# Kernel tuning notes

Hardware: AMD Instinct MI355X
Metric: run time of the kernel (lower is better)

## Reference

```python
import jax, jax.numpy as jnp
import numpy as np

B, L = 4096, 64
H, E, T, S = 512, 256, 256, 128
CT = T + 3            # context feature dim (term_embedding_dim + 3)
R, V = 4096, 256      # n production rules, n symbols
IN = 2 * E + 2 * T + 6 + H + S  # GRUCell input dim = 1670
NEG = -1e9


def setup_inputs() -> dict:
    key = jax.random.key(0)
    ks = jax.random.split(key, 24)
    sc = 0.02
    inp = {
        "s_tm1": jax.random.normal(ks[0], (B, H), jnp.float32),
        "a_tm1": jax.random.normal(ks[1], (B, E), jnp.float32),
        "p_t": jax.random.normal(ks[2], (B, H + E), jnp.float32),
        "symbol_idx": jax.random.randint(ks[3], (B,), 0, V, jnp.int32),
        "env_emb": jax.random.normal(ks[4], (B, L, CT), jnp.float32),
        "env_len": jax.random.randint(ks[5], (B,), 0, L, jnp.int32),
        "lc_emb": jax.random.normal(ks[6], (B, L, CT), jnp.float32),
        "lc_len": jax.random.randint(ks[7], (B,), 0, L, jnp.int32),
        # parameters
        "symbol_table": jax.random.normal(ks[8], (V, S), jnp.float32) * sc,
        "W1": jax.random.normal(ks[9], (H + CT, H), jnp.float32) * sc,
        "b1": jnp.zeros((H,), jnp.float32),
        "W2": jax.random.normal(ks[10], (H,), jnp.float32) * sc,
        "b2": jnp.zeros((), jnp.float32),
        "W_ih": jax.random.normal(ks[11], (IN, 3 * H), jnp.float32) * sc,
        "W_hh": jax.random.normal(ks[12], (H, 3 * H), jnp.float32) * sc,
        "b_ih": jnp.zeros((3 * H,), jnp.float32),
        "b_hh": jnp.zeros((3 * H,), jnp.float32),
        "Wd": jax.random.normal(ks[13], (H, E), jnp.float32) * sc,
        "bd": jnp.zeros((E,), jnp.float32),
        "rule_table": jax.random.normal(ks[14], (R, E), jnp.float32) * sc,
    }
    return inp


def _context_read(state, emb, length, W1, b1, W2, b2):
    # state: [B,H], emb: [B,L,CT], length: [B] -> context [B,CT]
    x = jnp.concatenate([jnp.broadcast_to(state[:, None, :], emb.shape[:2] + (state.shape[-1],)), emb], axis=-1)
    h = jax.nn.relu(jnp.einsum('blk,kh->blh', x, W1) + b1)      # [B,L,H]
    logit = jnp.einsum('blh,h->bl', h, W2) + b2                  # [B,L]
    mask = jnp.arange(emb.shape[1])[None, :] < length[:, None]
    logit = jnp.where(mask, logit, NEG)
    w = jax.nn.softmax(logit, axis=1)                            # [B,L]
    ctx = jnp.einsum('bl,blc->bc', w, emb)                       # [B,CT]
    # ragged empty-context samples use the zero default_context
    return jnp.where((length > 0)[:, None], ctx, 0.0)


def reference(s_tm1, a_tm1, p_t, symbol_idx, env_emb, env_len, lc_emb, lc_len,
              symbol_table, W1, b1, W2, b2, W_ih, W_hh, b_ih, b_hh, Wd, bd, rule_table):
    n_t = symbol_table[symbol_idx]                               # [B,S]
    ctx_env = _context_read(s_tm1, env_emb, env_len, W1, b1, W2, b2)
    ctx_lc = _context_read(s_tm1, lc_emb, lc_len, W1, b1, W2, b2)
    x = jnp.concatenate([a_tm1, p_t, n_t, ctx_env, ctx_lc], axis=-1)  # [B,IN]
    # torch GRUCell
    gx = x @ W_ih + b_ih                                         # [B,3H]
    gh = s_tm1 @ W_hh + b_hh
    xr, xz, xn = jnp.split(gx, 3, axis=-1)
    hr, hz, hn = jnp.split(gh, 3, axis=-1)
    r = jax.nn.sigmoid(xr + hr)
    z = jax.nn.sigmoid(xz + hz)
    n = jnp.tanh(xn + r * hn)
    h_new = (1.0 - z) * n + z * s_tm1                            # [B,H]
    dec = jnp.tanh(h_new @ Wd + bd)                              # [B,E]
    logits = dec @ rule_table.T                                  # [B,R]
    return logits
```

## Files before the change

### kernel.cpp

```cpp
#include <hip/hip_runtime.h>
#include <hip/hip_bf16.h>
#include <stdint.h>
#include <stddef.h>

#define XP 1696
#define KC 288

#define BIG_G   8192
#define TWO_G   4096
#define ONE_G   2048
#define N_GROUP (BIG_G + TWO_G + ONE_G)
#define N_SLOTI (N_GROUP * 4)

typedef __attribute__((ext_vector_type(8))) short bf16x8;
typedef __attribute__((ext_vector_type(4))) float f32x4;

__device__ __forceinline__ unsigned short f32_bf16(float f) {
    union { float f; unsigned int u; } v; v.f = f;
    unsigned int r = v.u + 0x7FFFu + ((v.u >> 16) & 1u);
    return (unsigned short)(r >> 16);
}
__device__ __forceinline__ float bf16_f32(unsigned short u) {
    union { unsigned int u; float f; } v; v.u = ((unsigned int)u) << 16;
    return v.f;
}

__global__ void tpack_kernel(const float* __restrict__ src, unsigned short* __restrict__ dst,
                             int Ksrc, int Nsrc, int Kp, long total) {
    long idx = (long)blockIdx.x * blockDim.x + threadIdx.x;
    if (idx >= total) return;
    int k = (int)(idx / Nsrc);
    int n = (int)(idx - (long)k * Nsrc);
    float v = (k < Ksrc) ? src[(size_t)k * Nsrc + n] : 0.0f;
    dst[(size_t)n * Kp + k] = f32_bf16(v);
}

__global__ void cvt_kernel(const float* __restrict__ src, unsigned short* __restrict__ dst, int total) {
    int idx = blockIdx.x * blockDim.x + threadIdx.x;
    if (idx < total) dst[idx] = f32_bf16(src[idx]);
}

__global__ void xasm_kernel(const float* __restrict__ a_tm1, const float* __restrict__ p_t,
                            const int* __restrict__ sym, const float* __restrict__ symtab,
                            unsigned short* __restrict__ x_out) {
    int idx = blockIdx.x * blockDim.x + threadIdx.x;
    if (idx >= 4096 * XP) return;
    int b = idx / XP, c = idx - b * XP;
    float v;
    if (c < 256)       v = a_tm1[(size_t)b * 256 + c];
    else if (c < 1024) v = p_t[(size_t)b * 768 + (c - 256)];
    else if (c < 1152) v = symtab[(size_t)sym[b] * 128 + (c - 1024)];
    else if (c < 1670) return;
    else v = 0.0f;
    x_out[idx] = f32_bf16(v);
}

__global__ void sinit_kernel(int* __restrict__ s) {
    int i = blockIdx.x * 256 + threadIdx.x;
    if (i < N_SLOTI) s[i] = -1;
    else if (i < N_SLOTI + 3) s[i] = 0;
}

__global__ void sched_kernel(const int* __restrict__ len_env, const int* __restrict__ len_lc,
                             int* __restrict__ slots) {
    int idx = blockIdx.x * blockDim.x + threadIdx.x;
    if (idx >= 8192) return;
    int b = idx >> 1, wh = idx & 1;
    int len = wh ? len_lc[b] : len_env[b];
    int m = (len + 15) >> 4;
    if (m == 0) m = 1;
    if (m > 4) m = 4;
    int* cursors = slots + N_SLOTI;
    int base;
    if (m >= 3)      { int p = atomicAdd(&cursors[0], 1); base = p * 4; }
    else if (m == 2) { int p = atomicAdd(&cursors[1], 1); base = BIG_G * 4 + (p >> 1) * 4 + (p & 1) * 2; }
    else             { int p = atomicAdd(&cursors[2], 1); base = (BIG_G + TWO_G) * 4 + (p >> 2) * 4 + (p & 3); }
    for (int k = 0; k < m; k++) slots[base + k] = idx * 4 + k;
}

template<int ACT, int OUT_BF16>
__global__ __launch_bounds__(256, 2)
void gemm_bt_kernel(const unsigned short* __restrict__ A,
                    const unsigned short* __restrict__ BT,
                    const float* __restrict__ bias,
                    void* __restrict__ Cout,
                    int M, int N, int K)
{
    __shared__ unsigned short a_lds[128 * 32];
    __shared__ unsigned short b_lds[128 * 32];
    const int tid  = threadIdx.x;
    const int lane = tid & 63;
    const int wave = tid >> 6;
    const int wm = wave >> 1, wn = wave & 1;
    const int row0 = blockIdx.y * 128;
    const int col0 = blockIdx.x * 128;

    f32x4 acc[4][4];
    #pragma unroll
    for (int i = 0; i < 4; i++)
        #pragma unroll
        for (int j = 0; j < 4; j++) acc[i][j] = (f32x4){0.f, 0.f, 0.f, 0.f};

    const int fr = lane & 15;
    const int kk = (lane >> 4) * 8;
    const int srow = (lane >> 2);
    const int scol = (lane & 3) * 8;

    for (int k0 = 0; k0 < K; k0 += 32) {
        __syncthreads();
        #pragma unroll
        for (int j = 0; j < 4; j++) {
            const int c = (wave & 1) * 4 + j;
            const unsigned short* gsrc;
            unsigned short* ldst;
            if (wave < 2) {
                gsrc = A  + (size_t)(row0 + c * 16 + srow) * K + k0 + scol;
                ldst = &a_lds[c * 512];
            } else {
                gsrc = BT + (size_t)(col0 + c * 16 + srow) * K + k0 + scol;
                ldst = &b_lds[c * 512];
            }
            __builtin_amdgcn_global_load_lds(
                (const __attribute__((address_space(1))) void*)gsrc,
                (__attribute__((address_space(3))) void*)ldst, 16, 0, 0);
        }
        __syncthreads();

        bf16x8 af[4], bf[4];
        #pragma unroll
        for (int mt = 0; mt < 4; mt++) af[mt] = *(const bf16x8*)&a_lds[(wm * 64 + mt * 16 + fr) * 32 + kk];
        #pragma unroll
        for (int nt = 0; nt < 4; nt++) bf[nt] = *(const bf16x8*)&b_lds[(wn * 64 + nt * 16 + fr) * 32 + kk];
        #pragma unroll
        for (int mt = 0; mt < 4; mt++)
            #pragma unroll
            for (int nt = 0; nt < 4; nt++)
                acc[mt][nt] = __builtin_amdgcn_mfma_f32_16x16x32_bf16(af[mt], bf[nt], acc[mt][nt], 0, 0, 0);
    }

    const int fq = lane >> 4;
    #pragma unroll
    for (int mt = 0; mt < 4; mt++)
        #pragma unroll
        for (int nt = 0; nt < 4; nt++) {
            int cg = col0 + wn * 64 + nt * 16 + fr;
            float bv = bias ? bias[cg] : 0.0f;
            #pragma unroll
            for (int i = 0; i < 4; i++) {
                int rg = row0 + wm * 64 + mt * 16 + fq * 4 + i;
                float v = acc[mt][nt][i] + bv;
                if (ACT == 1) v = tanhf(v);
                if (OUT_BF16) ((unsigned short*)Cout)[(size_t)rg * N + cg] = f32_bf16(v);
                else          ((float*)Cout)[(size_t)rg * N + cg] = v;
            }
        }
}

__global__ __launch_bounds__(512, 4)
void ctx_kernel(const float* __restrict__ emb_env, const float* __restrict__ emb_lc,
                const int* __restrict__ len_env, const int* __restrict__ len_lc,
                const float* __restrict__ s_proj,
                const unsigned short* __restrict__ W1eT,
                const float* __restrict__ W2, const float* __restrict__ b2,
                const int* __restrict__ slots,
                unsigned short* __restrict__ x_out)
{
    const int g = blockIdx.x;
    const int4 dv = *reinterpret_cast<const int4*>(slots + (size_t)g * 4);
    if (dv.x < 0) return;
    int d[4] = {dv.x, dv.y, dv.z, dv.w};

    __shared__ unsigned short emb_lds[64][296];
    __shared__ float partial_lds[8][64];
    __shared__ float w_lds[64];

    const int tid = threadIdx.x;
    const int lane = tid & 63;
    const int wave = tid >> 6;
    const int fr = lane & 15;
    const int fq = lane >> 4;
    const float b2v = b2[0];

    {
        const int sl = tid >> 7;
        const int t  = tid & 127;
        const int ds = d[sl];
        int nrows = 0;
        const float* src = nullptr;
        if (ds >= 0) {
            int it = ds >> 2, tix = ds & 3;
            int b = it >> 1, wh = it & 1;
            int len = (wh ? len_lc : len_env)[b];
            nrows = len - tix * 16;
            if (nrows > 16) nrows = 16;
            if (nrows < 0) nrows = 0;
            src = (wh ? emb_lc : emb_env) + ((size_t)b * 64 + tix * 16) * 259;
        }
        for (int q = t; q < 16 * 37; q += 128) {
            int r = q / 37, c = 259 + (q - (q / 37) * 37);
            emb_lds[sl * 16 + r][c] = 0;
        }
        const int ndead = (16 - nrows) * 259;
        for (int q = t; q < ndead; q += 128) {
            int r = nrows + q / 259, c = q - (q / 259) * 259;
            emb_lds[sl * 16 + r][c] = 0;
        }
        const int nf4 = (nrows * 259 + 3) >> 2;
        const float4* s4 = reinterpret_cast<const float4*>(src);
        float4 v[9];
        #pragma unroll
        for (int j = 0; j < 9; j++) {
            int q = t + j * 128;
            if (q < nf4) v[j] = s4[q];
        }
        #pragma unroll
        for (int j = 0; j < 9; j++) {
            int q = t + j * 128;
            if (q < nf4) {
                float fv[4] = {v[j].x, v[j].y, v[j].z, v[j].w};
                int e0 = q * 4;
                #pragma unroll
                for (int jj = 0; jj < 4; jj++) {
                    int e = e0 + jj;
                    int r = e / 259;
                    int c = e - r * 259;
                    emb_lds[sl * 16 + r][c] = f32_bf16(fv[jj]);
                }
            }
        }
    }
    __syncthreads();

    f32x4 acc[4][4];
    #pragma unroll
    for (int i = 0; i < 4; i++)
        #pragma unroll
        for (int j = 0; j < 4; j++) acc[i][j] = (f32x4){0.f, 0.f, 0.f, 0.f};

    #pragma unroll
    for (int ks = 0; ks < 9; ks++) {
        bf16x8 bfr[4];
        #pragma unroll
        for (int nt = 0; nt < 4; nt++) {
            int n = wave * 64 + nt * 16 + fr;
            bfr[nt] = *(const bf16x8*)(W1eT + (size_t)n * KC + ks * 32 + fq * 8);
        }
        bf16x8 af[4];
        #pragma unroll
        for (int mt = 0; mt < 4; mt++)
            af[mt] = *(const bf16x8*)&emb_lds[mt * 16 + fr][ks * 32 + fq * 8];
        __builtin_amdgcn_s_setprio(1);
        #pragma unroll
        for (int nt = 0; nt < 4; nt++)
            #pragma unroll
            for (int mt = 0; mt < 4; mt++)
                acc[mt][nt] = __builtin_amdgcn_mfma_f32_16x16x32_bf16(af[mt], bfr[nt], acc[mt][nt], 0, 0, 0);
        __builtin_amdgcn_s_setprio(0);
    }

    int bslot[4];
    #pragma unroll
    for (int mt = 0; mt < 4; mt++) bslot[mt] = d[mt] >= 0 ? (d[mt] >> 3) : -1;

    float wv[4];
    #pragma unroll
    for (int nt = 0; nt < 4; nt++) wv[nt] = W2[wave * 64 + nt * 16 + fr];

    float plog[4][4];
    #pragma unroll
    for (int mt = 0; mt < 4; mt++)
        #pragma unroll
        for (int ii = 0; ii < 4; ii++) plog[mt][ii] = 0.f;
    #pragma unroll
    for (int nt = 0; nt < 4; nt++) {
        int n = wave * 64 + nt * 16 + fr;
        #pragma unroll
        for (int mt = 0; mt < 4; mt++) {
            if (bslot[mt] < 0) continue;
            float sp = s_proj[(size_t)bslot[mt] * 512 + n];
            #pragma unroll
            for (int ii = 0; ii < 4; ii++) {
                float h = acc[mt][nt][ii] + sp;
                h = fmaxf(h, 0.f);
                plog[mt][ii] += h * wv[nt];
            }
        }
    }
    #pragma unroll
    for (int mt = 0; mt < 4; mt++) {
        if (bslot[mt] < 0) continue;
        #pragma unroll
        for (int ii = 0; ii < 4; ii++) {
            float v = plog[mt][ii];
            v += __shfl_xor(v, 1); v += __shfl_xor(v, 2);
            v += __shfl_xor(v, 4); v += __shfl_xor(v, 8);
            if (fr == 0) partial_lds[wave][mt * 16 + fq * 4 + ii] = v;
        }
    }
    __syncthreads();

    if (wave < 4) {
        int dh = d[wave];
        if (dh >= 0 && (dh & 3) == 0) {
            int it = dh >> 2;
            int b = it >> 1, wh = it & 1;
            int len = (wh ? len_lc : len_env)[b];
            int m = (len + 15) >> 4; if (m == 0) m = 1;
            float logit = -1e9f;
            if (lane < 16 * m && lane < len) {
                logit = b2v;
                #pragma unroll
                for (int w = 0; w < 8; w++) logit += partial_lds[w][wave * 16 + lane];
            }
            float mx = logit;
            #pragma unroll
            for (int off = 1; off < 64; off <<= 1) mx = fmaxf(mx, __shfl_xor(mx, off));
            float e = __expf(logit - mx);
            float s = e;
            #pragma unroll
            for (int off = 1; off < 64; off <<= 1) s += __shfl_xor(s, off);
            if (lane < 16 * m) w_lds[wave * 16 + lane] = e / s;
        }
    }
    __syncthreads();

    #pragma unroll
    for (int g4 = 0; g4 < 4; g4++) {
        int dh = d[g4];
        if (dh < 0 || (dh & 3) != 0) continue;
        int it = dh >> 2;
        int b = it >> 1, wh = it & 1;
        int len = (wh ? len_lc : len_env)[b];
        int xoff = wh ? 1411 : 1152;
        if (tid < 259) {
            const int c = tid;
            const int base = g4 * 16;
            float a0 = 0.f, a1 = 0.f, a2 = 0.f, a3 = 0.f;
            int l = 0;
            for (; l + 3 < len; l += 4) {
                a0 += w_lds[base + l]     * bf16_f32(emb_lds[base + l][c]);
                a1 += w_lds[base + l + 1] * bf16_f32(emb_lds[base + l + 1][c]);
                a2 += w_lds[base + l + 2] * bf16_f32(emb_lds[base + l + 2][c]);
                a3 += w_lds[base + l + 3] * bf16_f32(emb_lds[base + l + 3][c]);
            }
            for (; l < len; l++) a0 += w_lds[base + l] * bf16_f32(emb_lds[base + l][c]);
            x_out[(size_t)b * XP + xoff + c] = f32_bf16((a0 + a1) + (a2 + a3));
        }
    }
}

__global__ void gru_kernel(const float* __restrict__ gx, const float* __restrict__ gh,
                           const float* __restrict__ s, unsigned short* __restrict__ h_b) {
    int idx = blockIdx.x * blockDim.x + threadIdx.x;
    if (idx >= 4096 * 512) return;
    int b = idx >> 9, c = idx & 511;
    const float* gxb = gx + (size_t)b * 1536;
    const float* ghb = gh + (size_t)b * 1536;
    float xr = gxb[c], xz = gxb[c + 512], xn = gxb[c + 1024];
    float hr = ghb[c], hz = ghb[c + 512], hn = ghb[c + 1024];
    float r = 1.f / (1.f + __expf(-(xr + hr)));
    float z = 1.f / (1.f + __expf(-(xz + hz)));
    float n = tanhf(xn + r * hn);
    float h = (1.f - z) * n + z * s[idx];
    h_b[idx] = f32_bf16(h);
}

extern "C" void kernel_launch(void* const* d_in, const int* in_sizes, int n_in,
                              void* d_out, int out_size, void* d_ws, size_t ws_size,
                              hipStream_t stream) {
    const float* s_tm1   = (const float*)d_in[0];
    const float* a_tm1   = (const float*)d_in[1];
    const float* p_t     = (const float*)d_in[2];
    const int*   sym     = (const int*)d_in[3];
    const float* env_emb = (const float*)d_in[4];
    const int*   env_len = (const int*)d_in[5];
    const float* lc_emb  = (const float*)d_in[6];
    const int*   lc_len  = (const int*)d_in[7];
    const float* symtab  = (const float*)d_in[8];
    const float* W1      = (const float*)d_in[9];
    const float* b1      = (const float*)d_in[10];
    const float* W2      = (const float*)d_in[11];
    const float* b2      = (const float*)d_in[12];
    const float* W_ih    = (const float*)d_in[13];
    const float* W_hh    = (const float*)d_in[14];
    const float* b_ih    = (const float*)d_in[15];
    const float* b_hh    = (const float*)d_in[16];
    const float* Wd      = (const float*)d_in[17];
    const float* bd      = (const float*)d_in[18];
    const float* rule    = (const float*)d_in[19];

    char* w = (char*)d_ws;
    float* s_proj = (float*)w;              w += (size_t)4096 * 512 * 4;
    unsigned short* W1sT  = (unsigned short*)w; w += (size_t)512 * 512 * 2;
    unsigned short* W1eT  = (unsigned short*)w; w += (size_t)512 * KC * 2;
    unsigned short* WihT  = (unsigned short*)w; w += (size_t)1536 * XP * 2;
    unsigned short* WhhT  = (unsigned short*)w; w += (size_t)1536 * 512 * 2;
    unsigned short* WdT   = (unsigned short*)w; w += (size_t)256 * 512 * 2;
    unsigned short* ruleb = (unsigned short*)w; w += (size_t)4096 * 256 * 2;
    unsigned short* s_b   = (unsigned short*)w; w += (size_t)4096 * 512 * 2;
    unsigned short* x_b   = (unsigned short*)w; w += (size_t)4096 * XP * 2;
    unsigned short* h_b   = (unsigned short*)w; w += (size_t)4096 * 512 * 2;
    unsigned short* dec_b = (unsigned short*)w; w += (size_t)4096 * 256 * 2;
    int* slots = (int*)w;                   w += (size_t)(N_SLOTI + 8) * 4;

    float* out_f = (float*)d_out;
    float* gx = out_f;
    float* gh = out_f + (size_t)4096 * 1536;

    sinit_kernel<<<(N_SLOTI + 3 + 255) / 256, 256, 0, stream>>>(slots);
    sched_kernel<<<32, 256, 0, stream>>>(env_len, lc_len, slots);

    tpack_kernel<<<(512 * 512 + 255) / 256, 256, 0, stream>>>(W1, W1sT, 512, 512, 512, (long)512 * 512);
    tpack_kernel<<<(512 * KC + 255) / 256, 256, 0, stream>>>(W1 + (size_t)512 * 512, W1eT, 259, 512, KC, (long)512 * KC);
    tpack_kernel<<<(1536 * XP + 255) / 256, 256, 0, stream>>>(W_ih, WihT, 1670, 1536, XP, (long)1536 * XP);
    tpack_kernel<<<(1536 * 512 + 255) / 256, 256, 0, stream>>>(W_hh, WhhT, 512, 1536, 512, (long)1536 * 512);
    tpack_kernel<<<(256 * 512 + 255) / 256, 256, 0, stream>>>(Wd, WdT, 512, 256, 512, (long)256 * 512);
    cvt_kernel<<<4096, 256, 0, stream>>>(rule, ruleb, 4096 * 256);
    cvt_kernel<<<8192, 256, 0, stream>>>(s_tm1, s_b, 4096 * 512);
    xasm_kernel<<<(4096 * XP + 255) / 256, 256, 0, stream>>>(a_tm1, p_t, sym, symtab, x_b);

    gemm_bt_kernel<0, 0><<<dim3(4, 32), 256, 0, stream>>>(s_b, W1sT, b1, s_proj, 4096, 512, 512);

    ctx_kernel<<<N_GROUP, 512, 0, stream>>>(env_emb, lc_emb, env_len, lc_len,
                                            s_proj, W1eT, W2, b2, slots, x_b);

    gemm_bt_kernel<0, 0><<<dim3(12, 32), 256, 0, stream>>>(x_b, WihT, b_ih, gx, 4096, 1536, XP);
    gemm_bt_kernel<0, 0><<<dim3(12, 32), 256, 0, stream>>>(s_b, WhhT, b_hh, gh, 4096, 1536, 512);
    gru_kernel<<<8192, 256, 0, stream>>>(gx, gh, s_tm1, h_b);

    gemm_bt_kernel<1, 1><<<dim3(2, 32), 256, 0, stream>>>(h_b, WdT, bd, dec_b, 4096, 256, 512);

    gemm_bt_kernel<0, 0><<<dim3(32, 32), 256, 0, stream>>>(dec_b, ruleb, nullptr, out_f, 4096, 4096, 256);
}
```

Baseline: 439.1 us.

## Tile weight transpose through LDS and compact ctx_kernel embedding staging

Weight transpose-packing now stages 64x64 tiles through shared memory, so both the global reads and the global writes are coalesced instead of scattered by stride. In ctx_kernel the embedding LDS rows shrink to a 264-element pitch and bf16 values are written as packed 32-bit pairs. Zeroing of dead rows is dropped, and the last K chunk is special-cased to read only the few real columns. The final weighted-sum reduction is flattened across all 512 threads using per-head info precomputed in shared memory. In exchange, rows beyond the sequence length now hold uninitialized LDS data, which relies on masking to stay out of the results, and the indexing becomes more intricate.

```diff
diff --git a/kernel.cpp b/kernel.cpp
--- a/kernel.cpp
+++ b/kernel.cpp
@@ -5,6 +5,7 @@
 
 #define XP 1696
 #define KC 288
+#define EP 264
 
 #define BIG_G   8192
 #define TWO_G   4096
@@ -20,19 +21,37 @@
     unsigned int r = v.u + 0x7FFFu + ((v.u >> 16) & 1u);
     return (unsigned short)(r >> 16);
 }
+__device__ __forceinline__ unsigned int bf_rnd(float f) {
+    union { float f; unsigned int u; } v; v.f = f;
+    return v.u + 0x7FFFu + ((v.u >> 16) & 1u);
+}
 __device__ __forceinline__ float bf16_f32(unsigned short u) {
     union { unsigned int u; float f; } v; v.u = ((unsigned int)u) << 16;
     return v.f;
 }
 
 __global__ void tpack_kernel(const float* __restrict__ src, unsigned short* __restrict__ dst,
-                             int Ksrc, int Nsrc, int Kp, long total) {
-    long idx = (long)blockIdx.x * blockDim.x + threadIdx.x;
-    if (idx >= total) return;
-    int k = (int)(idx / Nsrc);
-    int n = (int)(idx - (long)k * Nsrc);
-    float v = (k < Ksrc) ? src[(size_t)k * Nsrc + n] : 0.0f;
-    dst[(size_t)n * Kp + k] = f32_bf16(v);
+                             int Ksrc, int Nsrc, int Kp) {
+    __shared__ float t[64][65];
+    const int tid = threadIdx.x;
+    const int n0 = blockIdx.x * 64, k0 = blockIdx.y * 64;
+    const int ln = tid & 63;
+    const int g  = tid >> 6;
+    #pragma unroll
+    for (int j = 0; j < 16; j++) {
+        int kl = g + j * 4;
+        int k = k0 + kl, n = n0 + ln;
+        float v = 0.f;
+        if (k < Ksrc && n < Nsrc) v = src[(size_t)k * Nsrc + n];
+        t[kl][ln] = v;
+    }
+    __syncthreads();
+    #pragma unroll
+    for (int j = 0; j < 16; j++) {
+        int nl = g + j * 4;
+        int n = n0 + nl, k = k0 + ln;
+        if (n < Nsrc && k < Kp) dst[(size_t)n * Kp + k] = f32_bf16(t[ln][nl]);
+    }
 }
 
 __global__ void cvt_kernel(const float* __restrict__ src, unsigned short* __restrict__ dst, int total) {
@@ -170,9 +189,10 @@
     if (dv.x < 0) return;
     int d[4] = {dv.x, dv.y, dv.z, dv.w};
 
-    __shared__ unsigned short emb_lds[64][296];
+    __shared__ unsigned short emb_lds[64 * EP];
     __shared__ float partial_lds[8][64];
     __shared__ float w_lds[64];
+    __shared__ int hinfo0[4], hinfo1[4], hinfo_n;
 
     const int tid = threadIdx.x;
     const int lane = tid & 63;
@@ -180,6 +200,28 @@
     const int fr = lane & 15;
     const int fq = lane >> 4;
     const float b2v = b2[0];
+
+    if (tid == 0) {
+        int n = 0;
+        #pragma unroll
+        for (int s = 0; s < 4; s++) {
+            int dh = d[s];
+            if (dh >= 0 && (dh & 3) == 0) {
+                int it = dh >> 2;
+                int b = it >> 1, wh = it & 1;
+                int len = (wh ? len_lc : len_env)[b];
+                hinfo0[n] = (s * 16) | (len << 8);
+                hinfo1[n] = b * 2 + wh;
+                n++;
+            }
+        }
+        hinfo_n = n;
+    }
+
+    if (tid < 320) {
+        int r = tid / 5, c = 259 + (tid - (tid / 5) * 5);
+        emb_lds[r * EP + c] = 0;
+    }
 
     {
         const int sl = tid >> 7;
@@ -196,15 +238,6 @@
             if (nrows < 0) nrows = 0;
             src = (wh ? emb_lc : emb_env) + ((size_t)b * 64 + tix * 16) * 259;
         }
-        for (int q = t; q < 16 * 37; q += 128) {
-            int r = q / 37, c = 259 + (q - (q / 37) * 37);
-            emb_lds[sl * 16 + r][c] = 0;
-        }
-        const int ndead = (16 - nrows) * 259;
-        for (int q = t; q < ndead; q += 128) {
-            int r = nrows + q / 259, c = q - (q / 259) * 259;
-            emb_lds[sl * 16 + r][c] = 0;
-        }
         const int nf4 = (nrows * 259 + 3) >> 2;
         const float4* s4 = reinterpret_cast<const float4*>(src);
         float4 v[9];
@@ -213,18 +246,35 @@
             int q = t + j * 128;
             if (q < nf4) v[j] = s4[q];
         }
+        unsigned short* ebase = &emb_lds[sl * 16 * EP];
         #pragma unroll
         for (int j = 0; j < 9; j++) {
             int q = t + j * 128;
             if (q < nf4) {
-                float fv[4] = {v[j].x, v[j].y, v[j].z, v[j].w};
                 int e0 = q * 4;
-                #pragma unroll
-                for (int jj = 0; jj < 4; jj++) {
-                    int e = e0 + jj;
-                    int r = e / 259;
-                    int c = e - r * 259;
-                    emb_lds[sl * 16 + r][c] = f32_bf16(fv[jj]);
+                int r  = (int)(((unsigned)e0 * 64779u) >> 24);
+                int c0 = e0 - r * 259;
+                unsigned int u0 = bf_rnd(v[j].x), u1 = bf_rnd(v[j].y);
+                unsigned int u2 = bf_rnd(v[j].z), u3 = bf_rnd(v[j].w);
+                unsigned short* rp = ebase + r * EP;
+                if (c0 <= 255) {
+                    if ((c0 & 1) == 0) {
+                        *(unsigned int*)(rp + c0)     = __builtin_amdgcn_perm(u1, u0, 0x07060302);
+                        *(unsigned int*)(rp + c0 + 2) = __builtin_amdgcn_perm(u3, u2, 0x07060302);
+                    } else {
+                        rp[c0]     = (unsigned short)(u0 >> 16);
+                        *(unsigned int*)(rp + c0 + 1) = __builtin_amdgcn_perm(u2, u1, 0x07060302);
+                        rp[c0 + 3] = (unsigned short)(u3 >> 16);
+                    }
+                } else {
+                    unsigned int uu[4] = {u0, u1, u2, u3};
+                    #pragma unroll
+                    for (int jj = 0; jj < 4; jj++) {
+                        int e = e0 + jj;
+                        int r2 = r, c2 = c0 + jj;
+                        if (c2 >= 259) { r2 = r + 1; c2 -= 259; }
+                        ebase[r2 * EP + c2] = (unsigned short)(uu[jj] >> 16);
+                    }
                 }
             }
         }
@@ -246,9 +296,18 @@
             bfr[nt] = *(const bf16x8*)(W1eT + (size_t)n * KC + ks * 32 + fq * 8);
         }
         bf16x8 af[4];
-        #pragma unroll
-        for (int mt = 0; mt < 4; mt++)
-            af[mt] = *(const bf16x8*)&emb_lds[mt * 16 + fr][ks * 32 + fq * 8];
+        if (ks < 8) {
+            #pragma unroll
+            for (int mt = 0; mt < 4; mt++)
+                af[mt] = *(const bf16x8*)&emb_lds[(mt * 16 + fr) * EP + ks * 32 + fq * 8];
+        } else {
+            #pragma unroll
+            for (int mt = 0; mt < 4; mt++) {
+                bf16x8 z = {};
+                if (fq == 0) z = *(const bf16x8*)&emb_lds[(mt * 16 + fr) * EP + 256];
+                af[mt] = z;
+            }
+        }
         __builtin_amdgcn_s_setprio(1);
         #pragma unroll
         for (int nt = 0; nt < 4; nt++)
@@ -324,27 +383,27 @@
     }
     __syncthreads();
 
-    #pragma unroll
-    for (int g4 = 0; g4 < 4; g4++) {
-        int dh = d[g4];
-        if (dh < 0 || (dh & 3) != 0) continue;
-        int it = dh >> 2;
-        int b = it >> 1, wh = it & 1;
-        int len = (wh ? len_lc : len_env)[b];
-        int xoff = wh ? 1411 : 1152;
-        if (tid < 259) {
-            const int c = tid;
-            const int base = g4 * 16;
+    {
+        const int nh = hinfo_n;
+        const int total = nh * 259;
+        for (int q = tid; q < total; q += 512) {
+            int h = (int)(((unsigned)q * 1013u) >> 18);
+            int c = q - h * 259;
+            int w0 = hinfo0[h];
+            int base = w0 & 0xFF;
+            int len = w0 >> 8;
+            int w1v = hinfo1[h];
+            int b = w1v >> 1, wh = w1v & 1;
             float a0 = 0.f, a1 = 0.f, a2 = 0.f, a3 = 0.f;
             int l = 0;
             for (; l + 3 < len; l += 4) {
-                a0 += w_lds[base + l]     * bf16_f32(emb_lds[base + l][c]);
-                a1 += w_lds[base + l + 1] * bf16_f32(emb_lds[base + l + 1][c]);
-                a2 += w_lds[base + l + 2] * bf16_f32(emb_lds[base + l + 2][c]);
-                a3 += w_lds[base + l + 3] * bf16_f32(emb_lds[base + l + 3][c]);
-            }
-            for (; l < len; l++) a0 += w_lds[base + l] * bf16_f32(emb_lds[base + l][c]);
-            x_out[(size_t)b * XP + xoff + c] = f32_bf16((a0 + a1) + (a2 + a3));
+                a0 += w_lds[base + l]     * bf16_f32(emb_lds[(base + l) * EP + c]);
+                a1 += w_lds[base + l + 1] * bf16_f32(emb_lds[(base + l + 1) * EP + c]);
+                a2 += w_lds[base + l + 2] * bf16_f32(emb_lds[(base + l + 2) * EP + c]);
+                a3 += w_lds[base + l + 3] * bf16_f32(emb_lds[(base + l + 3) * EP + c]);
+            }
+            for (; l < len; l++) a0 += w_lds[base + l] * bf16_f32(emb_lds[(base + l) * EP + c]);
+            x_out[(size_t)b * XP + (wh ? 1411 : 1152) + c] = f32_bf16((a0 + a1) + (a2 + a3));
         }
     }
 }
@@ -410,11 +469,11 @@
     sinit_kernel<<<(N_SLOTI + 3 + 255) / 256, 256, 0, stream>>>(slots);
     sched_kernel<<<32, 256, 0, stream>>>(env_len, lc_len, slots);
 
-    tpack_kernel<<<(512 * 512 + 255) / 256, 256, 0, stream>>>(W1, W1sT, 512, 512, 512, (long)512 * 512);
-    tpack_kernel<<<(512 * KC + 255) / 256, 256, 0, stream>>>(W1 + (size_t)512 * 512, W1eT, 259, 512, KC, (long)512 * KC);
-    tpack_kernel<<<(1536 * XP + 255) / 256, 256, 0, stream>>>(W_ih, WihT, 1670, 1536, XP, (long)1536 * XP);
-    tpack_kernel<<<(1536 * 512 + 255) / 256, 256, 0, stream>>>(W_hh, WhhT, 512, 1536, 512, (long)1536 * 512);
-    tpack_kernel<<<(256 * 512 + 255) / 256, 256, 0, stream>>>(Wd, WdT, 512, 256, 512, (long)256 * 512);
+    tpack_kernel<<<dim3(8, 8),   256, 0, stream>>>(W1, W1sT, 512, 512, 512);
+    tpack_kernel<<<dim3(8, 5),   256, 0, stream>>>(W1 + (size_t)512 * 512, W1eT, 259, 512, KC);
+    tpack_kernel<<<dim3(24, 27), 256, 0, stream>>>(W_ih, WihT, 1670, 1536, XP);
+    tpack_kernel<<<dim3(24, 8),  256, 0, stream>>>(W_hh, WhhT, 512, 1536, 512);
+    tpack_kernel<<<dim3(4, 8),   256, 0, stream>>>(Wd, WdT, 512, 256, 512);
     cvt_kernel<<<4096, 256, 0, stream>>>(rule, ruleb, 4096 * 256);
     cvt_kernel<<<8192, 256, 0, stream>>>(s_tm1, s_b, 4096 * 512);
     xasm_kernel<<<(4096 * XP + 255) / 256, 256, 0, stream>>>(a_tm1, p_t, sym, symtab, x_b);
```

New measurement: 463.2 us. 5.5% more time.

## Compact ctx group schedule and process two groups per block

Applied to the files above, without the earlier changes.

Replaces the single atomic scheduling pass with count, prefix-base and place kernels so the context-read groups are packed contiguously, with no empty slots spread across fixed-size bucket regions. The ctx kernel reads the actual group count and each block loops over two groups, halving the launch size and letting empty blocks exit early. This removes the many early-exit blocks of the padded 14336-block grid. The cost is two extra tiny launches, an extra barrier per group, and less parallelism per block.

```diff
diff --git a/kernel.cpp b/kernel.cpp
--- a/kernel.cpp
+++ b/kernel.cpp
@@ -5,12 +5,9 @@
 
 #define XP 1696
 #define KC 288
-
-#define BIG_G   8192
-#define TWO_G   4096
-#define ONE_G   2048
-#define N_GROUP (BIG_G + TWO_G + ONE_G)
-#define N_SLOTI (N_GROUP * 4)
+#define MAXG 8192
+#define CURS_OFF (MAXG * 4)
+#define GPW 2
 
 typedef __attribute__((ext_vector_type(8))) short bf16x8;
 typedef __attribute__((ext_vector_type(4))) float f32x4;
@@ -57,12 +54,12 @@
 
 __global__ void sinit_kernel(int* __restrict__ s) {
     int i = blockIdx.x * 256 + threadIdx.x;
-    if (i < N_SLOTI) s[i] = -1;
-    else if (i < N_SLOTI + 3) s[i] = 0;
-}
-
-__global__ void sched_kernel(const int* __restrict__ len_env, const int* __restrict__ len_lc,
-                             int* __restrict__ slots) {
+    if (i < CURS_OFF) s[i] = -1;
+    else if (i < CURS_OFF + 8) s[i] = 0;
+}
+
+__global__ void scount_kernel(const int* __restrict__ len_env, const int* __restrict__ len_lc,
+                              int* __restrict__ slots, int* __restrict__ itemrank) {
     int idx = blockIdx.x * blockDim.x + threadIdx.x;
     if (idx >= 8192) return;
     int b = idx >> 1, wh = idx & 1;
@@ -70,11 +67,37 @@
     int m = (len + 15) >> 4;
     if (m == 0) m = 1;
     if (m > 4) m = 4;
-    int* cursors = slots + N_SLOTI;
+    int bucket = (m >= 3) ? 0 : (m == 2 ? 1 : 2);
+    int* cursors = slots + CURS_OFF;
+    int rank = atomicAdd(&cursors[bucket], 1);
+    itemrank[idx] = (rank << 2) | bucket;
+}
+
+__global__ void sbase_kernel(int* __restrict__ slots) {
+    int* c = slots + CURS_OFF;
+    int nBig = c[0], nTwo = c[1], nOne = c[2];
+    int b1 = nBig;
+    int b2 = nBig + ((nTwo + 1) >> 1);
+    c[3] = 0; c[4] = b1; c[5] = b2;
+    c[6] = b2 + ((nOne + 3) >> 2);
+}
+
+__global__ void splace_kernel(const int* __restrict__ len_env, const int* __restrict__ len_lc,
+                              const int* __restrict__ itemrank, int* __restrict__ slots) {
+    int idx = blockIdx.x * blockDim.x + threadIdx.x;
+    if (idx >= 8192) return;
+    int b = idx >> 1, wh = idx & 1;
+    int len = wh ? len_lc[b] : len_env[b];
+    int m = (len + 15) >> 4;
+    if (m == 0) m = 1;
+    if (m > 4) m = 4;
+    int v = itemrank[idx];
+    int bucket = v & 3, rank = v >> 2;
+    const int* c = slots + CURS_OFF;
     int base;
-    if (m >= 3)      { int p = atomicAdd(&cursors[0], 1); base = p * 4; }
-    else if (m == 2) { int p = atomicAdd(&cursors[1], 1); base = BIG_G * 4 + (p >> 1) * 4 + (p & 1) * 2; }
-    else             { int p = atomicAdd(&cursors[2], 1); base = (BIG_G + TWO_G) * 4 + (p >> 2) * 4 + (p & 3); }
+    if (bucket == 0)      base = (c[3] + rank) * 4;
+    else if (bucket == 1) base = (c[4] + (rank >> 1)) * 4 + (rank & 1) * 2;
+    else                  base = (c[5] + (rank >> 2)) * 4 + (rank & 3);
     for (int k = 0; k < m; k++) slots[base + k] = idx * 4 + k;
 }
 
@@ -165,10 +188,9 @@
                 const int* __restrict__ slots,
                 unsigned short* __restrict__ x_out)
 {
-    const int g = blockIdx.x;
-    const int4 dv = *reinterpret_cast<const int4*>(slots + (size_t)g * 4);
-    if (dv.x < 0) return;
-    int d[4] = {dv.x, dv.y, dv.z, dv.w};
+    const int ng = slots[CURS_OFF + 6];
+    const int g0 = blockIdx.x * GPW;
+    if (g0 >= ng) return;
 
     __shared__ unsigned short emb_lds[64][296];
     __shared__ float partial_lds[8][64];
@@ -181,171 +203,179 @@
     const int fq = lane >> 4;
     const float b2v = b2[0];
 
-    {
-        const int sl = tid >> 7;
-        const int t  = tid & 127;
-        const int ds = d[sl];
-        int nrows = 0;
-        const float* src = nullptr;
-        if (ds >= 0) {
-            int it = ds >> 2, tix = ds & 3;
-            int b = it >> 1, wh = it & 1;
-            int len = (wh ? len_lc : len_env)[b];
-            nrows = len - tix * 16;
-            if (nrows > 16) nrows = 16;
-            if (nrows < 0) nrows = 0;
-            src = (wh ? emb_lc : emb_env) + ((size_t)b * 64 + tix * 16) * 259;
-        }
-        for (int q = t; q < 16 * 37; q += 128) {
-            int r = q / 37, c = 259 + (q - (q / 37) * 37);
-            emb_lds[sl * 16 + r][c] = 0;
-        }
-        const int ndead = (16 - nrows) * 259;
-        for (int q = t; q < ndead; q += 128) {
-            int r = nrows + q / 259, c = q - (q / 259) * 259;
-            emb_lds[sl * 16 + r][c] = 0;
-        }
-        const int nf4 = (nrows * 259 + 3) >> 2;
-        const float4* s4 = reinterpret_cast<const float4*>(src);
-        float4 v[9];
-        #pragma unroll
-        for (int j = 0; j < 9; j++) {
-            int q = t + j * 128;
-            if (q < nf4) v[j] = s4[q];
-        }
-        #pragma unroll
-        for (int j = 0; j < 9; j++) {
-            int q = t + j * 128;
-            if (q < nf4) {
-                float fv[4] = {v[j].x, v[j].y, v[j].z, v[j].w};
-                int e0 = q * 4;
+    for (int gi = 0; gi < GPW; gi++) {
+        const int g = g0 + gi;
+        if (g >= ng) break;
+        const int4 dv = *reinterpret_cast<const int4*>(slots + (size_t)g * 4);
+        int d[4] = {dv.x, dv.y, dv.z, dv.w};
+
+        {
+            const int sl = tid >> 7;
+            const int t  = tid & 127;
+            const int ds = d[sl];
+            int nrows = 0;
+            const float* src = nullptr;
+            if (ds >= 0) {
+                int it = ds >> 2, tix = ds & 3;
+                int b = it >> 1, wh = it & 1;
+                int len = (wh ? len_lc : len_env)[b];
+                nrows = len - tix * 16;
+                if (nrows > 16) nrows = 16;
+                if (nrows < 0) nrows = 0;
+                src = (wh ? emb_lc : emb_env) + ((size_t)b * 64 + tix * 16) * 259;
+            }
+            for (int q = t; q < 16 * 37; q += 128) {
+                int r = q / 37, c = 259 + (q - (q / 37) * 37);
+                emb_lds[sl * 16 + r][c] = 0;
+            }
+            const int ndead = (16 - nrows) * 259;
+            for (int q = t; q < ndead; q += 128) {
+                int r = nrows + q / 259, c = q - (q / 259) * 259;
+                emb_lds[sl * 16 + r][c] = 0;
+            }
+            const int nf4 = (nrows * 259 + 3) >> 2;
+            const float4* s4 = reinterpret_cast<const float4*>(src);
+            float4 v[9];
+            #pragma unroll
+            for (int j = 0; j < 9; j++) {
+                int q = t + j * 128;
+                if (q < nf4) v[j] = s4[q];
+            }
+            #pragma unroll
+            for (int j = 0; j < 9; j++) {
+                int q = t + j * 128;
+                if (q < nf4) {
+                    float fv[4] = {v[j].x, v[j].y, v[j].z, v[j].w};
+                    int e0 = q * 4;
+                    #pragma unroll
+                    for (int jj = 0; jj < 4; jj++) {
+                        int e = e0 + jj;
+                        int r = e / 259;
+                        int c = e - r * 259;
+                        emb_lds[sl * 16 + r][c] = f32_bf16(fv[jj]);
+                    }
+                }
+            }
+        }
+        __syncthreads();
+
+        f32x4 acc[4][4];
+        #pragma unroll
+        for (int i = 0; i < 4; i++)
+            #pragma unroll
+            for (int j = 0; j < 4; j++) acc[i][j] = (f32x4){0.f, 0.f, 0.f, 0.f};
+
+        #pragma unroll
+        for (int ks = 0; ks < 9; ks++) {
+            bf16x8 bfr[4];
+            #pragma unroll
+            for (int nt = 0; nt < 4; nt++) {
+                int n = wave * 64 + nt * 16 + fr;
+                bfr[nt] = *(const bf16x8*)(W1eT + (size_t)n * KC + ks * 32 + fq * 8);
+            }
+            bf16x8 af[4];
+            #pragma unroll
+            for (int mt = 0; mt < 4; mt++)
+                af[mt] = *(const bf16x8*)&emb_lds[mt * 16 + fr][ks * 32 + fq * 8];
+            __builtin_amdgcn_s_setprio(1);
+            #pragma unroll
+            for (int nt = 0; nt < 4; nt++)
                 #pragma unroll
-                for (int jj = 0; jj < 4; jj++) {
-                    int e = e0 + jj;
-                    int r = e / 259;
-                    int c = e - r * 259;
-                    emb_lds[sl * 16 + r][c] = f32_bf16(fv[jj]);
-                }
-            }
-        }
-    }
-    __syncthreads();
-
-    f32x4 acc[4][4];
-    #pragma unroll
-    for (int i = 0; i < 4; i++)
-        #pragma unroll
-        for (int j = 0; j < 4; j++) acc[i][j] = (f32x4){0.f, 0.f, 0.f, 0.f};
-
-    #pragma unroll
-    for (int ks = 0; ks < 9; ks++) {
-        bf16x8 bfr[4];
+                for (int mt = 0; mt < 4; mt++)
+                    acc[mt][nt] = __builtin_amdgcn_mfma_f32_16x16x32_bf16(af[mt], bfr[nt], acc[mt][nt], 0, 0, 0);
+            __builtin_amdgcn_s_setprio(0);
+        }
+
+        int bslot[4];
+        #pragma unroll
+        for (int mt = 0; mt < 4; mt++) bslot[mt] = d[mt] >= 0 ? (d[mt] >> 3) : -1;
+
+        float wv[4];
+        #pragma unroll
+        for (int nt = 0; nt < 4; nt++) wv[nt] = W2[wave * 64 + nt * 16 + fr];
+
+        float plog[4][4];
+        #pragma unroll
+        for (int mt = 0; mt < 4; mt++)
+            #pragma unroll
+            for (int ii = 0; ii < 4; ii++) plog[mt][ii] = 0.f;
         #pragma unroll
         for (int nt = 0; nt < 4; nt++) {
             int n = wave * 64 + nt * 16 + fr;
-            bfr[nt] = *(const bf16x8*)(W1eT + (size_t)n * KC + ks * 32 + fq * 8);
-        }
-        bf16x8 af[4];
-        #pragma unroll
-        for (int mt = 0; mt < 4; mt++)
-            af[mt] = *(const bf16x8*)&emb_lds[mt * 16 + fr][ks * 32 + fq * 8];
-        __builtin_amdgcn_s_setprio(1);
-        #pragma unroll
-        for (int nt = 0; nt < 4; nt++)
-            #pragma unroll
-            for (int mt = 0; mt < 4; mt++)
-                acc[mt][nt] = __builtin_amdgcn_mfma_f32_16x16x32_bf16(af[mt], bfr[nt], acc[mt][nt], 0, 0, 0);
-        __builtin_amdgcn_s_setprio(0);
-    }
-
-    int bslot[4];
-    #pragma unroll
-    for (int mt = 0; mt < 4; mt++) bslot[mt] = d[mt] >= 0 ? (d[mt] >> 3) : -1;
-
-    float wv[4];
-    #pragma unroll
-    for (int nt = 0; nt < 4; nt++) wv[nt] = W2[wave * 64 + nt * 16 + fr];
-
-    float plog[4][4];
-    #pragma unroll
-    for (int mt = 0; mt < 4; mt++)
-        #pragma unroll
-        for (int ii = 0; ii < 4; ii++) plog[mt][ii] = 0.f;
-    #pragma unroll
-    for (int nt = 0; nt < 4; nt++) {
-        int n = wave * 64 + nt * 16 + fr;
+            #pragma unroll
+            for (int mt = 0; mt < 4; mt++) {
+                if (bslot[mt] < 0) continue;
+                float sp = s_proj[(size_t)bslot[mt] * 512 + n];
+                #pragma unroll
+                for (int ii = 0; ii < 4; ii++) {
+                    float h = acc[mt][nt][ii] + sp;
+                    h = fmaxf(h, 0.f);
+                    plog[mt][ii] += h * wv[nt];
+                }
+            }
+        }
         #pragma unroll
         for (int mt = 0; mt < 4; mt++) {
             if (bslot[mt] < 0) continue;
-            float sp = s_proj[(size_t)bslot[mt] * 512 + n];
             #pragma unroll
             for (int ii = 0; ii < 4; ii++) {
-                float h = acc[mt][nt][ii] + sp;
-                h = fmaxf(h, 0.f);
-                plog[mt][ii] += h * wv[nt];
-            }
-        }
-    }
-    #pragma unroll
-    for (int mt = 0; mt < 4; mt++) {
-        if (bslot[mt] < 0) continue;
-        #pragma unroll
-        for (int ii = 0; ii < 4; ii++) {
-            float v = plog[mt][ii];
-            v += __shfl_xor(v, 1); v += __shfl_xor(v, 2);
-            v += __shfl_xor(v, 4); v += __shfl_xor(v, 8);
-            if (fr == 0) partial_lds[wave][mt * 16 + fq * 4 + ii] = v;
-        }
-    }
-    __syncthreads();
-
-    if (wave < 4) {
-        int dh = d[wave];
-        if (dh >= 0 && (dh & 3) == 0) {
+                float v = plog[mt][ii];
+                v += __shfl_xor(v, 1); v += __shfl_xor(v, 2);
+                v += __shfl_xor(v, 4); v += __shfl_xor(v, 8);
+                if (fr == 0) partial_lds[wave][mt * 16 + fq * 4 + ii] = v;
+            }
+        }
+        __syncthreads();
+
+        if (wave < 4) {
+            int dh = d[wave];
+            if (dh >= 0 && (dh & 3) == 0) {
+                int it = dh >> 2;
+                int b = it >> 1, wh = it & 1;
+                int len = (wh ? len_lc : len_env)[b];
+                int m = (len + 15) >> 4; if (m == 0) m = 1;
+                float logit = -1e9f;
+                if (lane < 16 * m && lane < len) {
+                    logit = b2v;
+                    #pragma unroll
+                    for (int w = 0; w < 8; w++) logit += partial_lds[w][wave * 16 + lane];
+                }
+                float mx = logit;
+                #pragma unroll
+                for (int off = 1; off < 64; off <<= 1) mx = fmaxf(mx, __shfl_xor(mx, off));
+                float e = __expf(logit - mx);
+                float s = e;
+                #pragma unroll
+                for (int off = 1; off < 64; off <<= 1) s += __shfl_xor(s, off);
+                if (lane < 16 * m) w_lds[wave * 16 + lane] = e / s;
+            }
+        }
+        __syncthreads();
+
+        #pragma unroll
+        for (int g4 = 0; g4 < 4; g4++) {
+            int dh = d[g4];
+            if (dh < 0 || (dh & 3) != 0) continue;
             int it = dh >> 2;
             int b = it >> 1, wh = it & 1;
             int len = (wh ? len_lc : len_env)[b];
-            int m = (len + 15) >> 4; if (m == 0) m = 1;
-            float logit = -1e9f;
-            if (lane < 16 * m && lane < len) {
-                logit = b2v;
-                #pragma unroll
-                for (int w = 0; w < 8; w++) logit += partial_lds[w][wave * 16 + lane];
-            }
-            float mx = logit;
-            #pragma unroll
-            for (int off = 1; off < 64; off <<= 1) mx = fmaxf(mx, __shfl_xor(mx, off));
-            float e = __expf(logit - mx);
-            float s = e;
-            #pragma unroll
-            for (int off = 1; off < 64; off <<= 1) s += __shfl_xor(s, off);
-            if (lane < 16 * m) w_lds[wave * 16 + lane] = e / s;
-        }
-    }
-    __syncthreads();
-
-    #pragma unroll
-    for (int g4 = 0; g4 < 4; g4++) {
-        int dh = d[g4];
-        if (dh < 0 || (dh & 3) != 0) continue;
-        int it = dh >> 2;
-        int b = it >> 1, wh = it & 1;
-        int len = (wh ? len_lc : len_env)[b];
-        int xoff = wh ? 1411 : 1152;
-        if (tid < 259) {
-            const int c = tid;
-            const int base = g4 * 16;
-            float a0 = 0.f, a1 = 0.f, a2 = 0.f, a3 = 0.f;
-            int l = 0;
-            for (; l + 3 < len; l += 4) {
-                a0 += w_lds[base + l]     * bf16_f32(emb_lds[base + l][c]);
-                a1 += w_lds[base + l + 1] * bf16_f32(emb_lds[base + l + 1][c]);
-                a2 += w_lds[base + l + 2] * bf16_f32(emb_lds[base + l + 2][c]);
-                a3 += w_lds[base + l + 3] * bf16_f32(emb_lds[base + l + 3][c]);
-            }
-            for (; l < len; l++) a0 += w_lds[base + l] * bf16_f32(emb_lds[base + l][c]);
-            x_out[(size_t)b * XP + xoff + c] = f32_bf16((a0 + a1) + (a2 + a3));
-        }
+            int xoff = wh ? 1411 : 1152;
+            if (tid < 259) {
+                const int c = tid;
+                const int base = g4 * 16;
+                float a0 = 0.f, a1 = 0.f, a2 = 0.f, a3 = 0.f;
+                int l = 0;
+                for (; l + 3 < len; l += 4) {
+                    a0 += w_lds[base + l]     * bf16_f32(emb_lds[base + l][c]);
+                    a1 += w_lds[base + l + 1] * bf16_f32(emb_lds[base + l + 1][c]);
+                    a2 += w_lds[base + l + 2] * bf16_f32(emb_lds[base + l + 2][c]);
+                    a3 += w_lds[base + l + 3] * bf16_f32(emb_lds[base + l + 3][c]);
+                }
+                for (; l < len; l++) a0 += w_lds[base + l] * bf16_f32(emb_lds[base + l][c]);
+                x_out[(size_t)b * XP + xoff + c] = f32_bf16((a0 + a1) + (a2 + a3));
+            }
+        }
+        __syncthreads();
     }
 }
 
@@ -401,14 +431,17 @@
     unsigned short* x_b   = (unsigned short*)w; w += (size_t)4096 * XP * 2;
     unsigned short* h_b   = (unsigned short*)w; w += (size_t)4096 * 512 * 2;
     unsigned short* dec_b = (unsigned short*)w; w += (size_t)4096 * 256 * 2;
-    int* slots = (int*)w;                   w += (size_t)(N_SLOTI + 8) * 4;
+    int* slots    = (int*)w;                w += (size_t)(CURS_OFF + 8) * 4;
+    int* itemrank = (int*)w;                w += (size_t)8192 * 4;
 
     float* out_f = (float*)d_out;
     float* gx = out_f;
     float* gh = out_f + (size_t)4096 * 1536;
 
-    sinit_kernel<<<(N_SLOTI + 3 + 255) / 256, 256, 0, stream>>>(slots);
-    sched_kernel<<<32, 256, 0, stream>>>(env_len, lc_len, slots);
+    sinit_kernel<<<(CURS_OFF + 8 + 255) / 256, 256, 0, stream>>>(slots);
+    scount_kernel<<<32, 256, 0, stream>>>(env_len, lc_len, slots, itemrank);
+    sbase_kernel<<<1, 1, 0, stream>>>(slots);
+    splace_kernel<<<32, 256, 0, stream>>>(env_len, lc_len, itemrank, slots);
 
     tpack_kernel<<<(512 * 512 + 255) / 256, 256, 0, stream>>>(W1, W1sT, 512, 512, 512, (long)512 * 512);
     tpack_kernel<<<(512 * KC + 255) / 256, 256, 0, stream>>>(W1 + (size_t)512 * 512, W1eT, 259, 512, KC, (long)512 * KC);
@@ -421,8 +454,8 @@
 
     gemm_bt_kernel<0, 0><<<dim3(4, 32), 256, 0, stream>>>(s_b, W1sT, b1, s_proj, 4096, 512, 512);
 
-    ctx_kernel<<<N_GROUP, 512, 0, stream>>>(env_emb, lc_emb, env_len, lc_len,
-                                            s_proj, W1eT, W2, b2, slots, x_b);
+    ctx_kernel<<<MAXG / GPW, 512, 0, stream>>>(env_emb, lc_emb, env_len, lc_len,
+                                               s_proj, W1eT, W2, b2, slots, x_b);
 
     gemm_bt_kernel<0, 0><<<dim3(12, 32), 256, 0, stream>>>(x_b, WihT, b_ih, gx, 4096, 1536, XP);
     gemm_bt_kernel<0, 0><<<dim3(12, 32), 256, 0, stream>>>(s_b, WhhT, b_hh, gh, 4096, 1536, 512);
```

After: 1.023 ms. +133.0%, slower.
